# Performance work log

Measured on AMD Instinct MI355X. Metric: run time of the kernel, lower is better.

## Reference

```python
import jax, jax.numpy as jnp
import numpy as np

B, D, H = 16, 512, 8
MA, MR = 2048, 256  # padded max atoms / residues per graph
EPS = 1e-5


def _counts():
    ca = 1024 + (np.arange(B) * 97) % 1024   # atoms per graph
    cr = 128 + (np.arange(B) * 37) % 128     # residues per graph
    return ca, cr


def to_dense(x, batch, M):
    """PyG to_dense_batch: flat [N, D] + sorted batch ids -> [B, M, D] padded + mask."""
    N = x.shape[0]
    counts = jax.ops.segment_sum(jnp.ones(N, jnp.int32), batch, num_segments=B)
    starts = jnp.concatenate([jnp.zeros(1, counts.dtype), jnp.cumsum(counts)[:-1]])
    pos = jnp.arange(N, dtype=jnp.int32) - starts[batch]
    dense = jnp.zeros((B, M, x.shape[1]), x.dtype).at[batch, pos].set(x)
    mask = jnp.zeros((B, M), bool).at[batch, pos].set(True)
    return dense, mask, batch, pos


def mha(q, k, v, in_w, in_b, out_w, out_b, key_valid):
    """torch nn.MultiheadAttention (batch_first, eval) with key_padding_mask = ~key_valid."""
    Lq, Lk = q.shape[1], k.shape[1]
    dh = D // H
    wq, wk, wv = in_w[:D], in_w[D:2 * D], in_w[2 * D:]
    bq, bk, bv = in_b[:D], in_b[D:2 * D], in_b[2 * D:]
    qh = (q @ wq.T + bq).reshape(B, Lq, H, dh)
    kh = (k @ wk.T + bk).reshape(B, Lk, H, dh)
    vh = (v @ wv.T + bv).reshape(B, Lk, H, dh)
    scores = jnp.einsum('bqhd,bkhd->bhqk', qh, kh) / jnp.sqrt(jnp.asarray(dh, q.dtype))
    scores = jnp.where(key_valid[:, None, None, :], scores, jnp.asarray(-1e9, scores.dtype))
    attn = jax.nn.softmax(scores, axis=-1)
    out = jnp.einsum('bhqk,bkhd->bqhd', attn, vh).reshape(B, Lq, D)
    return out @ out_w.T + out_b


def layernorm(x, g, b):
    m = x.mean(-1, keepdims=True)
    v = ((x - m) ** 2).mean(-1, keepdims=True)
    return (x - m) * jax.lax.rsqrt(v + EPS) * g + b


def setup_inputs() -> dict:
    key = jax.random.key(0)
    ks = jax.random.split(key, 8)
    ca, cr = _counts()
    Na, Nr = int(ca.sum()), int(cr.sum())
    s = 0.02
    return {
        'atom_node': jax.random.normal(ks[0], (Na, D), jnp.float32),
        'res_node': jax.random.normal(ks[1], (Nr, D), jnp.float32),
        'r2a_in_w': jax.random.normal(ks[2], (3 * D, D), jnp.float32) * s,
        'r2a_in_b': jnp.zeros((3 * D,), jnp.float32),
        'r2a_out_w': jax.random.normal(ks[3], (D, D), jnp.float32) * s,
        'r2a_out_b': jnp.zeros((D,), jnp.float32),
        'a2r_in_w': jax.random.normal(ks[4], (3 * D, D), jnp.float32) * s,
        'a2r_in_b': jnp.zeros((3 * D,), jnp.float32),
        'a2r_out_w': jax.random.normal(ks[5], (D, D), jnp.float32) * s,
        'a2r_out_b': jnp.zeros((D,), jnp.float32),
        'atom_ln_g': jnp.ones((D,), jnp.float32),
        'atom_ln_b': jnp.zeros((D,), jnp.float32),
        'res_ln_g': jnp.ones((D,), jnp.float32),
        'res_ln_b': jnp.zeros((D,), jnp.float32),
        'atom_batch': jnp.asarray(np.repeat(np.arange(B), ca), jnp.int32),
        'res_batch': jnp.asarray(np.repeat(np.arange(B), cr), jnp.int32),
    }


def reference(atom_node, res_node, r2a_in_w, r2a_in_b, r2a_out_w, r2a_out_b,
              a2r_in_w, a2r_in_b, a2r_out_w, a2r_out_b,
              atom_ln_g, atom_ln_b, res_ln_g, res_ln_b,
              atom_batch, res_batch):
    atom_d, atom_mask, ab, ap = to_dense(atom_node, atom_batch, MA)
    res_d, res_mask, rb, rp = to_dense(res_node, res_batch, MR)
    # res2atom: atoms attend over residues; atom2res: residues attend over (updated) atoms
    atom_upd = mha(atom_d, res_d, res_d, r2a_in_w, r2a_in_b, r2a_out_w, r2a_out_b, res_mask)
    res_upd = mha(res_d, atom_upd, atom_upd, a2r_in_w, a2r_in_b, a2r_out_w, a2r_out_b, atom_mask)
    atom_out = layernorm(atom_upd, atom_ln_g, atom_ln_b)[ab, ap] + atom_node
    res_out = layernorm(res_upd, res_ln_g, res_ln_b)[rb, rp] + res_node
    return atom_out, res_out
```

## Files before the change

kernel.cpp:

```cpp
#include <hip/hip_runtime.h>
#include <hip/hip_bf16.h>
#include <math.h>

#define DD 512
#define NA_TOT 22904
#define NR_TOT 2904
#define MPAD_A 22960
#define MPAD_R 2960

__constant__ int c_aoff[17] = {0,1024,2145,3363,4678,6090,7599,9205,10908,12708,
                               14605,16599,17666,18830,20091,21449,22904};
__constant__ int c_roff[17] = {0,128,293,495,734,882,1067,1289,1420,1588,
                               1793,2035,2186,2374,2599,2733,2904};
__constant__ int c_apad[17] = {0,1024,2152,3376,4696,6112,7624,9232,10936,12736,
                               14640,16640,17712,18880,20144,21504,22960};
__constant__ int c_rpad[17] = {0,128,296,504,744,896,1088,1312,1448,1616,
                               1824,2072,2224,2416,2648,2784,2960};

typedef __attribute__((ext_vector_type(8))) short short8;
typedef __attribute__((ext_vector_type(4))) float f32x4;
typedef __attribute__((ext_vector_type(4))) unsigned short ushort4v;

__device__ __forceinline__ unsigned short f2bf(float f) {
  __hip_bfloat16 h = __float2bfloat16(f);
  return *reinterpret_cast<unsigned short*>(&h);
}
__device__ __forceinline__ float bf2f(unsigned short u) {
  union { unsigned int i; float f; } c; c.i = ((unsigned int)u) << 16; return c.f;
}
__device__ __forceinline__ float wred_sum(float x){
#pragma unroll
  for (int o = 32; o > 0; o >>= 1) x += __shfl_xor(x, o, 64);
  return x;
}

__device__ __forceinline__ void gl_lds16(const unsigned short* g, unsigned short* l) {
  __builtin_amdgcn_global_load_lds(
      (const __attribute__((address_space(1))) unsigned int*)g,
      (__attribute__((address_space(3))) unsigned int*)l, 16, 0, 0);
}

__global__ __launch_bounds__(256) void cvt5(
    const float* __restrict__ s0, const float* __restrict__ s1,
    const float* __restrict__ s2, const float* __restrict__ s3,
    const float* __restrict__ s4,
    unsigned short* __restrict__ d0, unsigned short* __restrict__ d1,
    unsigned short* __restrict__ d2, unsigned short* __restrict__ d3,
    unsigned short* __restrict__ d4,
    int n0, int n1, int n2, int n3, int n4)
{
  const float* s; unsigned short* d; int n;
  switch (blockIdx.y) {
    case 0: s = s0; d = d0; n = n0; break;
    case 1: s = s1; d = d1; n = n1; break;
    case 2: s = s2; d = d2; n = n2; break;
    case 3: s = s3; d = d3; n = n3; break;
    default: s = s4; d = d4; n = n4; break;
  }
  const int i = (blockIdx.x * 256 + threadIdx.x) * 4;
  if (i < n) {
    const float4 v = *reinterpret_cast<const float4*>(s + i);
    ushort4v o = { f2bf(v.x), f2bf(v.y), f2bf(v.z), f2bf(v.w) };
    *reinterpret_cast<ushort4v*>(d + i) = o;
  }
}

__global__ __launch_bounds__(256) void mkmap(int* __restrict__ mapA,
                                             int* __restrict__ mapR)
{
  const int pm = blockIdx.x * 256 + threadIdx.x;
  if (pm < MPAD_A) {
    int b = 0;
#pragma unroll
    for (int i = 1; i < 16; ++i) if (pm >= c_apad[i]) b = i;
    const int rel = pm - c_apad[b];
    const int L = c_aoff[b+1] - c_aoff[b];
    mapA[pm] = c_aoff[b] + min(rel, L - 1);
  }
  if (pm < MPAD_R) {
    int b = 0;
#pragma unroll
    for (int i = 1; i < 16; ++i) if (pm >= c_rpad[i]) b = i;
    const int rel = pm - c_rpad[b];
    const int L = c_roff[b+1] - c_roff[b];
    mapR[pm] = c_roff[b] + min(rel, L - 1);
  }
}

struct GSeg {
  const void* X; const unsigned short* W; const float* bias;
  unsigned short* Y; const int* map;
  int M; int ldY; int mtiles; int flags;
};
struct GSeg4 { GSeg s[4]; };

__global__ __launch_bounds__(256) void gemm_multi(GSeg4 P, int mtpx)
{
  __shared__ unsigned short SMEM[2*128*64];
  unsigned short* Xs = SMEM;
  unsigned short* Ws = SMEM + 128*64;
  const GSeg sg = P.s[blockIdx.y];
  const int xcd = blockIdx.x & 7, g = blockIdx.x >> 3;
  const int mt = xcd + 8 * (g % mtpx);
  const int nt = g / mtpx;
  if (mt >= sg.mtiles) return;
  const int m0 = mt * 128, n0 = nt * 128;
  const int INF32 = sg.flags & 1, OUTT = sg.flags & 2, REMAP = sg.flags & 4;
  const int tid = threadIdx.x, lane = tid & 63, w = tid >> 6;
  const int la = lane & 15, lg = lane >> 4;
  const int wm = (w & 1) * 64, wn = (w >> 1) * 64;
  const int w64 = w * 64;

  f32x4 acc[4][4];
#pragma unroll
  for (int i = 0; i < 4; ++i)
#pragma unroll
    for (int j = 0; j < 4; ++j) acc[i][j] = (f32x4){0.f,0.f,0.f,0.f};

  int elA[4][2], elB[4][2];
#pragma unroll
  for (int i = 0; i < 4; ++i)
#pragma unroll
    for (int kc = 0; kc < 2; ++kc) {
      { const int r = wm + i*16 + la;
        elA[i][kc] = r*64 + ((kc*32 + lg*8) ^ ((r & 7) << 3)); }
      { const int r = wn + i*16 + la;
        elB[i][kc] = r*64 + ((kc*32 + lg*8) ^ ((r & 7) << 3)); }
    }

  int srow[4];
#pragma unroll
  for (int p = 0; p < 4; ++p) {
    const int slot = p*256 + tid;
    const int rg = min(m0 + (slot >> 3), sg.M - 1);
    srow[p] = REMAP ? sg.map[rg] : rg;
  }

  for (int kb = 0; kb < DD; kb += 64) {
    __syncthreads();
#pragma unroll
    for (int p = 0; p < 4; ++p) {
      const int slot = p*256 + tid;
      const int row = slot >> 3, cg = slot & 7;
      const int col = kb + ((cg ^ (row & 7)) << 3);
      gl_lds16(sg.W + (size_t)(n0 + row) * DD + col, &Ws[(p*256 + w64) * 8]);
    }
    if (INF32) {
      const float* X = (const float*)sg.X;
#pragma unroll
      for (int p = 0; p < 4; ++p) {
        const int slot = p*256 + tid;
        const int row = slot >> 3, cg = slot & 7;
        const int col = kb + ((cg ^ (row & 7)) << 3);
        const float* src = X + (size_t)srow[p] * DD + col;
        const float4 v0 = *reinterpret_cast<const float4*>(src);
        const float4 v1 = *reinterpret_cast<const float4*>(src + 4);
        short8 pk;
        pk[0] = (short)f2bf(v0.x); pk[1] = (short)f2bf(v0.y);
        pk[2] = (short)f2bf(v0.z); pk[3] = (short)f2bf(v0.w);
        pk[4] = (short)f2bf(v1.x); pk[5] = (short)f2bf(v1.y);
        pk[6] = (short)f2bf(v1.z); pk[7] = (short)f2bf(v1.w);
        *reinterpret_cast<short8*>(&Xs[slot * 8]) = pk;
      }
    } else {
      const unsigned short* X = (const unsigned short*)sg.X;
#pragma unroll
      for (int p = 0; p < 4; ++p) {
        const int slot = p*256 + tid;
        const int row = slot >> 3, cg = slot & 7;
        const int col = kb + ((cg ^ (row & 7)) << 3);
        gl_lds16(X + (size_t)srow[p] * DD + col, &Xs[(p*256 + w64) * 8]);
      }
    }
    __syncthreads();

    short8 af[4][2], bfm[4][2];
#pragma unroll
    for (int i = 0; i < 4; ++i)
#pragma unroll
      for (int kc = 0; kc < 2; ++kc) {
        af[i][kc]  = *reinterpret_cast<const short8*>(&Xs[elA[i][kc]]);
        bfm[i][kc] = *reinterpret_cast<const short8*>(&Ws[elB[i][kc]]);
      }
#pragma unroll
    for (int kc = 0; kc < 2; ++kc)
#pragma unroll
      for (int i = 0; i < 4; ++i)
#pragma unroll
        for (int j = 0; j < 4; ++j)
          acc[i][j] = __builtin_amdgcn_mfma_f32_16x16x32_bf16(af[i][kc], bfm[j][kc], acc[i][j], 0, 0, 0);
  }

  __syncthreads();
  unsigned short* Cs = SMEM;
  if (!OUTT) {
#pragma unroll
    for (int j = 0; j < 4; ++j) {
      const int n = wn + j*16 + la;
      const float bj = sg.bias[n0 + n];
#pragma unroll
      for (int i = 0; i < 4; ++i) {
        const int mb = wm + i*16 + lg*4;
#pragma unroll
        for (int r = 0; r < 4; ++r) {
          const int m = mb + r;
          Cs[m*128 + (((n >> 3) ^ (m & 7)) << 3) + (n & 7)] = f2bf(acc[i][j][r] + bj);
        }
      }
    }
    __syncthreads();
#pragma unroll
    for (int p = 0; p < 8; ++p) {
      const int sid = p*256 + tid;
      const int row = sid >> 4, s = sid & 15;
      if (m0 + row < sg.M) {
        const short8 v = *reinterpret_cast<const short8*>(&Cs[row*128 + ((s ^ (row & 7)) << 3)]);
        *reinterpret_cast<short8*>(sg.Y + (size_t)(m0 + row)*sg.ldY + n0 + s*8) = v;
      }
    }
  } else {
#pragma unroll
    for (int j = 0; j < 4; ++j) {
      const int n = wn + j*16 + la;
      const float bj = sg.bias[n0 + n];
#pragma unroll
      for (int i = 0; i < 4; ++i) {
        const int mb = wm + i*16 + lg*4;
#pragma unroll
        for (int r = 0; r < 4; ++r) {
          const int m = mb + r;
          Cs[n*128 + (((m >> 3) ^ (n & 7)) << 3) + (m & 7)] = f2bf(acc[i][j][r] + bj);
        }
      }
    }
    __syncthreads();
#pragma unroll
    for (int p = 0; p < 8; ++p) {
      const int sid = p*256 + tid;
      const int row = sid >> 4, s = sid & 15;
      if (m0 + s*8 < sg.M) {
        const short8 v = *reinterpret_cast<const short8*>(&Cs[row*128 + ((s ^ (row & 7)) << 3)]);
        *reinterpret_cast<short8*>(sg.Y + (size_t)(n0 + row)*sg.ldY + m0 + s*8) = v;
      }
    }
  }
}

template<int SWAP>
__global__ __launch_bounds__(256, 4) void attn_v7(const unsigned short* __restrict__ Q,
                                                  const unsigned short* __restrict__ K,
                                                  const unsigned short* __restrict__ VT,
                                                  unsigned short* __restrict__ O, int ldvt)
{
  __shared__ unsigned short Ks[2][64*64];
  __shared__ unsigned short Vs[2][64*64];
  __shared__ unsigned short Pl[4][16*64];
  const int* qo  = SWAP ? c_roff : c_aoff;
  const int* ko  = SWAP ? c_aoff : c_roff;
  const int* kop = SWAP ? c_apad : c_rpad;
  const int b = blockIdx.x >> 3, h = blockIdx.x & 7;
  const int Lq = qo[b+1]-qo[b], Lk = ko[b+1]-ko[b];
  const int padL = kop[b+1]-kop[b];
  const int q0b = blockIdx.y * 64;
  if (q0b >= Lq) return;
  const int tid = threadIdx.x, w = tid >> 6, lane = tid & 63;
  const int la = lane & 15, lg = lane >> 4;
  const int q0 = q0b + w*16;
  const unsigned short* Qb  = Q  + (size_t)qo[b]*DD + h*64;
  const unsigned short* Kb  = K  + (size_t)kop[b]*DD + h*64;
  const unsigned short* VTb = VT + (size_t)(h*64)*ldvt + kop[b];

  short8 qf[2];
  {
    const int qrow = min(q0 + la, Lq - 1);
    qf[0] = *reinterpret_cast<const short8*>(Qb + (size_t)qrow*DD + lg*8);
    qf[1] = *reinterpret_cast<const short8*>(Qb + (size_t)qrow*DD + 32 + lg*8);
  }

  f32x4 acc[4];
#pragma unroll
  for (int j = 0; j < 4; ++j) acc[j] = (f32x4){0.f,0.f,0.f,0.f};
  float lsum[4] = {0.f,0.f,0.f,0.f};

  const int nkc = (Lk + 63) >> 6;

#define STAGE(bi, kc_)                                                          \
  {                                                                             \
    const int kbase_ = (kc_) * 64;                                              \
    _Pragma("unroll")                                                           \
    for (int p = 0; p < 2; ++p) {                                               \
      const int slot = p*256 + tid;                                             \
      const int row = slot >> 3, cg = slot & 7;                                 \
      const int srow = min(kbase_ + row, padL - 1);                             \
      gl_lds16(Kb + (size_t)srow * DD + ((cg ^ (row & 7)) << 3),                \
               &Ks[bi][(p*256 + w*64) * 8]);                                    \
    }                                                                           \
    _Pragma("unroll")                                                           \
    for (int p = 0; p < 2; ++p) {                                               \
      const int slot = p*256 + tid;                                             \
      const int row = slot >> 3, cg = slot & 7;                                 \
      const int col = min(kbase_ + ((cg ^ (row & 7)) << 3), padL - 8);          \
      gl_lds16(VTb + (size_t)row * ldvt + col, &Vs[bi][(p*256 + w*64) * 8]);    \
    }                                                                           \
  }

  STAGE(0, 0);
  __syncthreads();

  for (int kc = 0; kc < nkc; ++kc) {
    const int bi = kc & 1;
    if (kc + 1 < nkc) STAGE(bi ^ 1, kc + 1);
    const int kbase = kc * 64;

    f32x4 S[4];
#pragma unroll
    for (int j = 0; j < 4; ++j) {
      const int row = j*16 + la;
      const short8 kf0 = *reinterpret_cast<const short8*>(
          &Ks[bi][row*64 + ((lg*8) ^ ((row & 7) << 3))]);
      const short8 kf1 = *reinterpret_cast<const short8*>(
          &Ks[bi][row*64 + ((32 + lg*8) ^ ((row & 7) << 3))]);
      f32x4 s = (f32x4){0.f,0.f,0.f,0.f};
      s = __builtin_amdgcn_mfma_f32_16x16x32_bf16(qf[0], kf0, s, 0, 0, 0);
      s = __builtin_amdgcn_mfma_f32_16x16x32_bf16(qf[1], kf1, s, 0, 0, 0);
      S[j] = s;
    }

#pragma unroll
    for (int j = 0; j < 4; ++j) {
      const bool ok = (kbase + j*16 + la) < Lk;
#pragma unroll
      for (int r = 0; r < 4; ++r) {
        const float p = ok ? __expf(S[j][r] * 0.125f) : 0.f;
        S[j][r] = p;
        lsum[r] += p;
      }
    }

#pragma unroll
    for (int r = 0; r < 4; ++r) {
      const int prow = lg*4 + r;
#pragma unroll
      for (int j = 0; j < 4; ++j)
        Pl[w][prow*64 + ((j*16 + la) ^ ((prow & 7) << 3))] = f2bf(S[j][r]);
    }
    __builtin_amdgcn_wave_barrier();
    const short8 pf0 = *reinterpret_cast<const short8*>(
        &Pl[w][la*64 + ((lg*8) ^ ((la & 7) << 3))]);
    const short8 pf1 = *reinterpret_cast<const short8*>(
        &Pl[w][la*64 + ((32 + lg*8) ^ ((la & 7) << 3))]);

#pragma unroll
    for (int j = 0; j < 4; ++j) {
      const int d = j*16 + la;
      const short8 vf0 = *reinterpret_cast<const short8*>(
          &Vs[bi][d*64 + ((lg*8) ^ ((d & 7) << 3))]);
      const short8 vf1 = *reinterpret_cast<const short8*>(
          &Vs[bi][d*64 + ((32 + lg*8) ^ ((d & 7) << 3))]);
      acc[j] = __builtin_amdgcn_mfma_f32_16x16x32_bf16(pf0, vf0, acc[j], 0, 0, 0);
      acc[j] = __builtin_amdgcn_mfma_f32_16x16x32_bf16(pf1, vf1, acc[j], 0, 0, 0);
    }
    __syncthreads();
  }

#pragma unroll
  for (int msk = 1; msk <= 8; msk <<= 1)
#pragma unroll
    for (int r = 0; r < 4; ++r) lsum[r] += __shfl_xor(lsum[r], msk, 64);

#pragma unroll
  for (int r = 0; r < 4; ++r) {
    const float inv = 1.f / lsum[r];
    const int prow = lg*4 + r;
#pragma unroll
    for (int j = 0; j < 4; ++j)
      Pl[w][prow*64 + ((j*16 + la) ^ ((prow & 7) << 3))] = f2bf(acc[j][r] * inv);
  }
  __builtin_amdgcn_wave_barrier();
#pragma unroll
  for (int p = 0; p < 2; ++p) {
    const int sid = p*64 + lane;
    const int row = sid >> 3, s = sid & 7;
    const int qrow = q0 + row;
    if (qrow < Lq) {
      const short8 v = *reinterpret_cast<const short8*>(
          &Pl[w][row*64 + ((s ^ (row & 7)) << 3)]);
      *reinterpret_cast<short8*>(O + (size_t)(qo[b] + qrow)*DD + h*64 + s*8) = v;
    }
  }
#undef STAGE
}

__global__ __launch_bounds__(256) void ln_res(const unsigned short* __restrict__ Ub,
    float* __restrict__ Yout,
    const float* __restrict__ atom_node, const float* __restrict__ res_node,
    const float* __restrict__ ag, const float* __restrict__ ab,
    const float* __restrict__ rg, const float* __restrict__ rb)
{
  const int row = blockIdx.x * 4 + (threadIdx.x >> 6);
  const int lane = threadIdx.x & 63;
  if (row >= NA_TOT + NR_TOT) return;
  const float* g; const float* bb; const float* resid;
  if (row < NA_TOT) { g = ag; bb = ab; resid = atom_node + (size_t)row * DD; }
  else { g = rg; bb = rb; resid = res_node + (size_t)(row - NA_TOT) * DD; }
  const short8 xb = *reinterpret_cast<const short8*>(Ub + (size_t)row*DD + lane*8);
  float xv[8];
#pragma unroll
  for (int i = 0; i < 8; ++i) xv[i] = bf2f((unsigned short)xb[i]);
  float s = 0.f;
#pragma unroll
  for (int i = 0; i < 8; ++i) s += xv[i];
  s = wred_sum(s);
  const float mean = s * (1.f/512.f);
  float vs = 0.f;
#pragma unroll
  for (int i = 0; i < 8; ++i) { const float d = xv[i] - mean; vs = fmaf(d, d, vs); }
  vs = wred_sum(vs) * (1.f/512.f);
  const float inv = rsqrtf(vs + 1e-5f);
  const float4 g0 = *reinterpret_cast<const float4*>(g + lane*8);
  const float4 g1 = *reinterpret_cast<const float4*>(g + lane*8 + 4);
  const float4 b0 = *reinterpret_cast<const float4*>(bb + lane*8);
  const float4 b1 = *reinterpret_cast<const float4*>(bb + lane*8 + 4);
  const float4 r0 = *reinterpret_cast<const float4*>(resid + lane*8);
  const float4 r1 = *reinterpret_cast<const float4*>(resid + lane*8 + 4);
  float4 o0, o1;
  o0.x = (xv[0]-mean)*inv*g0.x + b0.x + r0.x;
  o0.y = (xv[1]-mean)*inv*g0.y + b0.y + r0.y;
  o0.z = (xv[2]-mean)*inv*g0.z + b0.z + r0.z;
  o0.w = (xv[3]-mean)*inv*g0.w + b0.w + r0.w;
  o1.x = (xv[4]-mean)*inv*g1.x + b1.x + r1.x;
  o1.y = (xv[5]-mean)*inv*g1.y + b1.y + r1.y;
  o1.z = (xv[6]-mean)*inv*g1.z + b1.z + r1.z;
  o1.w = (xv[7]-mean)*inv*g1.w + b1.w + r1.w;
  float* y = Yout + (size_t)row * DD + lane*8;
  *reinterpret_cast<float4*>(y)     = o0;
  *reinterpret_cast<float4*>(y + 4) = o1;
}

extern "C" void kernel_launch(void* const* d_in, const int* in_sizes, int n_in,
                              void* d_out, int out_size, void* d_ws, size_t ws_size,
                              hipStream_t stream) {
  (void)in_sizes; (void)n_in; (void)out_size; (void)ws_size;
  const float* atom_node = (const float*)d_in[0];
  const float* res_node  = (const float*)d_in[1];
  const float* r2a_in_w  = (const float*)d_in[2];
  const float* r2a_in_b  = (const float*)d_in[3];
  const float* r2a_out_w = (const float*)d_in[4];
  const float* r2a_out_b = (const float*)d_in[5];
  const float* a2r_in_w  = (const float*)d_in[6];
  const float* a2r_in_b  = (const float*)d_in[7];
  const float* a2r_out_w = (const float*)d_in[8];
  const float* a2r_out_b = (const float*)d_in[9];
  const float* atom_ln_g = (const float*)d_in[10];
  const float* atom_ln_b = (const float*)d_in[11];
  const float* res_ln_g  = (const float*)d_in[12];
  const float* res_ln_b  = (const float*)d_in[13];

  float* out = (float*)d_out;
  unsigned short* wsb = (unsigned short*)d_ws;
  const size_t NAD = (size_t)NA_TOT * DD;
  const size_t NRD = (size_t)NR_TOT * DD;
  const size_t PAD = (size_t)MPAD_A * DD;
  const size_t PRD = (size_t)MPAD_R * DD;
  unsigned short* slab1  = wsb;
  unsigned short* slab2  = wsb + PAD;
  unsigned short* updb   = wsb + 2*PAD;
  unsigned short* res_bf = wsb + 2*PAD + NAD + NRD;
  unsigned short* K1     = res_bf + NRD;
  unsigned short* V1T    = K1 + PRD;
  unsigned short* Q2     = V1T + PRD;
  unsigned short* O2     = Q2 + NRD;
  unsigned short* wbf    = O2 + NRD;
  unsigned short* w_r2a_in  = wbf;
  unsigned short* w_r2a_out = wbf +  786432;
  unsigned short* w_a2r_in  = wbf + 1048576;
  unsigned short* w_a2r_out = wbf + 1835008;
  int* mapA = (int*)(wbf + 2097152);
  int* mapR = mapA + MPAD_A;
  unsigned short* Q1  = slab1;
  unsigned short* O1  = slab2;
  unsigned short* K2  = slab1;
  unsigned short* V2T = slab2;

  const dim3 blk(256);

  mkmap<<<dim3((MPAD_A + 255)/256), blk, 0, stream>>>(mapA, mapR);
  cvt5<<<dim3(1452, 5), blk, 0, stream>>>(
      r2a_in_w, r2a_out_w, a2r_in_w, a2r_out_w, res_node,
      w_r2a_in, w_r2a_out, w_a2r_in, w_a2r_out, res_bf,
      786432, 262144, 786432, 262144, (int)NRD);

  {
    GSeg4 A;
    A.s[0] = { atom_node, w_r2a_in,          r2a_in_b,        Q1,  nullptr, NA_TOT, 512,    179, 1 };
    A.s[1] = { res_bf,    w_r2a_in + 262144, r2a_in_b + 512,  K1,  mapR,    MPAD_R, 512,    24,  4 };
    A.s[2] = { res_bf,    w_r2a_in + 524288, r2a_in_b + 1024, V1T, mapR,    MPAD_R, MPAD_R, 24,  6 };
    A.s[3] = { res_bf,    w_a2r_in,          a2r_in_b,        Q2,  nullptr, NR_TOT, 512,    23,  0 };
    gemm_multi<<<dim3(736, 4), blk, 0, stream>>>(A, 23);
  }
  attn_v7<0><<<dim3(128, 32), blk, 0, stream>>>(Q1, K1, V1T, O1, MPAD_R);
  {
    GSeg4 B;
    B.s[0] = { O1, w_r2a_out, r2a_out_b, updb, nullptr, NA_TOT, 512, 179, 0 };
    B.s[1] = B.s[0]; B.s[2] = B.s[0]; B.s[3] = B.s[0];
    gemm_multi<<<dim3(736, 1), blk, 0, stream>>>(B, 23);
  }
  {
    GSeg4 C;
    C.s[0] = { updb, w_a2r_in + 262144, a2r_in_b + 512,  K2,  mapA, MPAD_A, 512,    180, 4 };
    C.s[1] = { updb, w_a2r_in + 524288, a2r_in_b + 1024, V2T, mapA, MPAD_A, MPAD_A, 180, 6 };
    C.s[2] = C.s[0]; C.s[3] = C.s[0];
    gemm_multi<<<dim3(736, 2), blk, 0, stream>>>(C, 23);
  }
  attn_v7<1><<<dim3(128, 4), blk, 0, stream>>>(Q2, K2, V2T, O2, MPAD_A);
  {
    GSeg4 E;
    E.s[0] = { O2, w_a2r_out, a2r_out_b, updb + NAD, nullptr, NR_TOT, 512, 23, 0 };
    E.s[1] = E.s[0]; E.s[2] = E.s[0]; E.s[3] = E.s[0];
    gemm_multi<<<dim3(96, 1), blk, 0, stream>>>(E, 3);
  }
  ln_res<<<dim3((NA_TOT + NR_TOT + 3) / 4), blk, 0, stream>>>(
      updb, out, atom_node, res_node, atom_ln_g, atom_ln_b, res_ln_g, res_ln_b);
}
```

Before: 214.8 us.

## Double-buffer LDS tiles in gemm_multi to overlap loads with MFMA

Doubles the shared-memory footprint of the projection GEMM so the next K-slice of X and W is prefetched into a second buffer while MFMAs run on the current one. For fp32 inputs the loads go into registers first and are converted and written to LDS after the compute. This removes one barrier per K step and hides global-load latency. The cost is 64 KB of LDS per block and extra registers for the prefetched fp32 data, both of which can lower occupancy.

```diff
diff --git a/kernel.cpp b/kernel.cpp
--- a/kernel.cpp
+++ b/kernel.cpp
@@ -96,9 +96,11 @@
 
 __global__ __launch_bounds__(256) void gemm_multi(GSeg4 P, int mtpx)
 {
-  __shared__ unsigned short SMEM[2*128*64];
-  unsigned short* Xs = SMEM;
-  unsigned short* Ws = SMEM + 128*64;
+  __shared__ unsigned short SMEM[4*128*64];
+  unsigned short* const X0 = SMEM;
+  unsigned short* const W0 = SMEM + 8192;
+  unsigned short* const X1 = SMEM + 16384;
+  unsigned short* const W1 = SMEM + 24576;
   const GSeg sg = P.s[blockIdx.y];
   const int xcd = blockIdx.x & 7, g = blockIdx.x >> 3;
   const int mt = xcd + 8 * (g % mtpx);
@@ -135,63 +137,95 @@
     const int rg = min(m0 + (slot >> 3), sg.M - 1);
     srow[p] = REMAP ? sg.map[rg] : rg;
   }
-
-  for (int kb = 0; kb < DD; kb += 64) {
+  int scg[4], srw[4];
+#pragma unroll
+  for (int p = 0; p < 4; ++p) {
+    const int slot = p*256 + tid;
+    srw[p] = slot >> 3;
+    scg[p] = ((slot & 7) ^ (srw[p] & 7)) << 3;
+  }
+
+  float4 xr[4][2];
+
+#define STAGE_W(DST, kb_)                                                       \
+  _Pragma("unroll")                                                             \
+  for (int p = 0; p < 4; ++p)                                                   \
+    gl_lds16(sg.W + (size_t)(n0 + srw[p]) * DD + (kb_) + scg[p],                \
+             &(DST)[(p*256 + w64) * 8]);
+
+#define STAGE_XB(DST, kb_)                                                      \
+  _Pragma("unroll")                                                             \
+  for (int p = 0; p < 4; ++p)                                                   \
+    gl_lds16((const unsigned short*)sg.X + (size_t)srow[p] * DD + (kb_) + scg[p],\
+             &(DST)[(p*256 + w64) * 8]);
+
+#define LOAD_XF(kb_)                                                            \
+  _Pragma("unroll")                                                             \
+  for (int p = 0; p < 4; ++p) {                                                 \
+    const float* src = (const float*)sg.X + (size_t)srow[p] * DD + (kb_) + scg[p];\
+    xr[p][0] = *reinterpret_cast<const float4*>(src);                           \
+    xr[p][1] = *reinterpret_cast<const float4*>(src + 4);                       \
+  }
+
+#define WRITE_XF(DST)                                                           \
+  _Pragma("unroll")                                                             \
+  for (int p = 0; p < 4; ++p) {                                                 \
+    short8 pk;                                                                  \
+    pk[0] = (short)f2bf(xr[p][0].x); pk[1] = (short)f2bf(xr[p][0].y);           \
+    pk[2] = (short)f2bf(xr[p][0].z); pk[3] = (short)f2bf(xr[p][0].w);           \
+    pk[4] = (short)f2bf(xr[p][1].x); pk[5] = (short)f2bf(xr[p][1].y);           \
+    pk[6] = (short)f2bf(xr[p][1].z); pk[7] = (short)f2bf(xr[p][1].w);           \
+    *reinterpret_cast<short8*>(&(DST)[(p*256 + tid) * 8]) = pk;                 \
+  }
+
+#define COMPUTE(XB, WB)                                                         \
+  {                                                                             \
+    short8 af[4][2], bfm[4][2];                                                 \
+    _Pragma("unroll")                                                           \
+    for (int i = 0; i < 4; ++i)                                                 \
+      _Pragma("unroll")                                                         \
+      for (int kc = 0; kc < 2; ++kc) {                                          \
+        af[i][kc]  = *reinterpret_cast<const short8*>(&(XB)[elA[i][kc]]);       \
+        bfm[i][kc] = *reinterpret_cast<const short8*>(&(WB)[elB[i][kc]]);       \
+      }                                                                         \
+    _Pragma("unroll")                                                           \
+    for (int kc = 0; kc < 2; ++kc)                                              \
+      _Pragma("unroll")                                                         \
+      for (int i = 0; i < 4; ++i)                                               \
+        _Pragma("unroll")                                                       \
+        for (int j = 0; j < 4; ++j)                                             \
+          acc[i][j] = __builtin_amdgcn_mfma_f32_16x16x32_bf16(af[i][kc], bfm[j][kc], acc[i][j], 0, 0, 0); \
+  }
+
+  if (INF32) { LOAD_XF(0); WRITE_XF(X0); }
+  else       { STAGE_XB(X0, 0); }
+  STAGE_W(W0, 0);
+  __syncthreads();
+
+#pragma unroll
+  for (int t = 0; t < 4; ++t) {
+    const int kb1 = t*128 + 64;
+    if (INF32) { LOAD_XF(kb1); } else { STAGE_XB(X1, kb1); }
+    STAGE_W(W1, kb1);
+    COMPUTE(X0, W0);
+    if (INF32) { WRITE_XF(X1); }
     __syncthreads();
-#pragma unroll
-    for (int p = 0; p < 4; ++p) {
-      const int slot = p*256 + tid;
-      const int row = slot >> 3, cg = slot & 7;
-      const int col = kb + ((cg ^ (row & 7)) << 3);
-      gl_lds16(sg.W + (size_t)(n0 + row) * DD + col, &Ws[(p*256 + w64) * 8]);
-    }
-    if (INF32) {
-      const float* X = (const float*)sg.X;
-#pragma unroll
-      for (int p = 0; p < 4; ++p) {
-        const int slot = p*256 + tid;
-        const int row = slot >> 3, cg = slot & 7;
-        const int col = kb + ((cg ^ (row & 7)) << 3);
-        const float* src = X + (size_t)srow[p] * DD + col;
-        const float4 v0 = *reinterpret_cast<const float4*>(src);
-        const float4 v1 = *reinterpret_cast<const float4*>(src + 4);
-        short8 pk;
-        pk[0] = (short)f2bf(v0.x); pk[1] = (short)f2bf(v0.y);
-        pk[2] = (short)f2bf(v0.z); pk[3] = (short)f2bf(v0.w);
-        pk[4] = (short)f2bf(v1.x); pk[5] = (short)f2bf(v1.y);
-        pk[6] = (short)f2bf(v1.z); pk[7] = (short)f2bf(v1.w);
-        *reinterpret_cast<short8*>(&Xs[slot * 8]) = pk;
-      }
-    } else {
-      const unsigned short* X = (const unsigned short*)sg.X;
-#pragma unroll
-      for (int p = 0; p < 4; ++p) {
-        const int slot = p*256 + tid;
-        const int row = slot >> 3, cg = slot & 7;
-        const int col = kb + ((cg ^ (row & 7)) << 3);
-        gl_lds16(X + (size_t)srow[p] * DD + col, &Xs[(p*256 + w64) * 8]);
-      }
-    }
+    const int kb2 = t*128 + 128;
+    if (kb2 < DD) {
+      if (INF32) { LOAD_XF(kb2); } else { STAGE_XB(X0, kb2); }
+      STAGE_W(W0, kb2);
+    }
+    COMPUTE(X1, W1);
+    if (INF32 && kb2 < DD) { WRITE_XF(X0); }
     __syncthreads();
-
-    short8 af[4][2], bfm[4][2];
-#pragma unroll
-    for (int i = 0; i < 4; ++i)
-#pragma unroll
-      for (int kc = 0; kc < 2; ++kc) {
-        af[i][kc]  = *reinterpret_cast<const short8*>(&Xs[elA[i][kc]]);
-        bfm[i][kc] = *reinterpret_cast<const short8*>(&Ws[elB[i][kc]]);
-      }
-#pragma unroll
-    for (int kc = 0; kc < 2; ++kc)
-#pragma unroll
-      for (int i = 0; i < 4; ++i)
-#pragma unroll
-        for (int j = 0; j < 4; ++j)
-          acc[i][j] = __builtin_amdgcn_mfma_f32_16x16x32_bf16(af[i][kc], bfm[j][kc], acc[i][j], 0, 0, 0);
-  }
-
-  __syncthreads();
+  }
+
+#undef STAGE_W
+#undef STAGE_XB
+#undef LOAD_XF
+#undef WRITE_XF
+#undef COMPUTE
+
   unsigned short* Cs = SMEM;
   if (!OUTT) {
 #pragma unroll
```

After: 214.3 us. No clear change (-0.2%).
